# Optimization experiments

Measured on AMD Instinct MI355X. Metric: run time of the kernel, lower is better.

Reference implementation:

```python
import jax, jax.numpy as jnp
import numpy as np

NUM_HEADS = 4
NUM_POINTS = 8


def setup_inputs() -> dict:
    key0 = jax.random.key(0)
    ks = jax.random.split(key0, 14)
    B, S, N, D, C = 1, 6, 10000, 4, 128
    Hf, Wf = 46, 80
    M = Hf * Wf
    HP2 = NUM_HEADS * NUM_POINTS * 2
    HP = NUM_HEADS * NUM_POINTS
    inp = {
        "query": jax.random.normal(ks[0], (B, N, C), jnp.float32),
        "key": jax.random.normal(ks[1], (S, M, B, C), jnp.float32),
        "value": jax.random.normal(ks[2], (S, M, B, C), jnp.float32),
        "query_pos": jax.random.normal(ks[3], (B, N, C), jnp.float32),
        "reference_points_cam": jax.random.uniform(ks[4], (S, B, N, D, 2), jnp.float32),
        "Wv": jax.random.normal(ks[5], (C, C), jnp.float32) * 0.02,
        "bv": jnp.zeros((C,), jnp.float32),
        "Wo": jax.random.normal(ks[6], (C, HP2), jnp.float32) * 0.02,
        "bo": jax.random.normal(ks[7], (HP2,), jnp.float32) * 0.5,
        "Wa": jax.random.normal(ks[8], (C, HP), jnp.float32) * 0.02,
        "ba": jnp.zeros((HP,), jnp.float32),
        "Wp": jax.random.normal(ks[9], (C, C), jnp.float32) * 0.02,
        "bp": jnp.zeros((C,), jnp.float32),
        "spatial_shapes": np.array([[Hf, Wf]], dtype=np.int64),
        "bev_mask": jax.random.uniform(ks[10], (S, B, N, D)) < 0.3,
    }
    return inp


def _bilinear_sample(value_hw, loc, Hf, Wf):
    # value_hw: [BS, H, Hf*Wf, Dh]; loc: [BS, L, H, P, 2] normalized to [0,1]
    # grid_sample(align_corners=False, padding=zeros) semantics: ix = x*W - 0.5
    x = loc[..., 0] * Wf - 0.5
    y = loc[..., 1] * Hf - 0.5
    x0 = jnp.floor(x)
    y0 = jnp.floor(y)
    lx = x - x0
    ly = y - y0
    x0i = x0.astype(jnp.int32)
    y0i = y0.astype(jnp.int32)

    BS, L, H, P = x.shape
    Dh = value_hw.shape[-1]

    def gat(xi, yi):
        valid = (xi >= 0) & (xi < Wf) & (yi >= 0) & (yi < Hf)
        idx = jnp.clip(yi, 0, Hf - 1) * Wf + jnp.clip(xi, 0, Wf - 1)  # [BS,L,H,P]
        idx_t = idx.transpose(0, 2, 1, 3).reshape(BS, H, L * P)
        v = jnp.take_along_axis(value_hw, idx_t[..., None], axis=2)  # [BS,H,L*P,Dh]
        v = v.reshape(BS, H, L, P, Dh)
        return v * valid.transpose(0, 2, 1, 3)[..., None]

    def wt(w):  # [BS,L,H,P] -> [BS,H,L,P,1]
        return w.transpose(0, 2, 1, 3)[..., None]

    out = (gat(x0i, y0i) * wt((1 - lx) * (1 - ly))
           + gat(x0i + 1, y0i) * wt(lx * (1 - ly))
           + gat(x0i, y0i + 1) * wt((1 - lx) * ly)
           + gat(x0i + 1, y0i + 1) * wt(lx * ly))
    return out  # [BS,H,L,P,Dh]


def _deform_attn(q, val, ref, Hf, Wf, Wv, bv, Wo, bo, Wa, ba):
    # q: [BS,L,C], val: [BS,M,C], ref: [BS,L,D,2]
    BS, L, C = q.shape
    Dh = C // NUM_HEADS
    D = ref.shape[2]
    value_p = (val @ Wv + bv).reshape(BS, -1, NUM_HEADS, Dh)
    value_hw = value_p.transpose(0, 2, 1, 3)  # [BS,H,M,Dh]

    off = (q @ Wo + bo).reshape(BS, L, NUM_HEADS, NUM_POINTS, 2)
    attw = jax.nn.softmax((q @ Wa + ba).reshape(BS, L, NUM_HEADS, NUM_POINTS), axis=-1)

    normalizer = jnp.array([Wf, Hf], dtype=q.dtype)  # (x_norm, y_norm)
    off = off / normalizer
    # split points into (points_per_Z, num_Z_anchors) and add per-anchor reference
    off = off.reshape(BS, L, NUM_HEADS, NUM_POINTS // D, D, 2)
    loc = ref[:, :, None, None, :, :] + off  # [BS,L,H,P//D,D,2]
    loc = loc.reshape(BS, L, NUM_HEADS, NUM_POINTS, 2)

    sampled = _bilinear_sample(value_hw, loc, Hf, Wf)  # [BS,H,L,P,Dh]
    out = jnp.einsum('bhlpd,blhp->blhd', sampled, attw)
    return out.reshape(BS, L, C)


def reference(query, key, value, query_pos, reference_points_cam,
              Wv, bv, Wo, bo, Wa, ba, Wp, bp, spatial_shapes, bev_mask):
    B, N, C = query.shape
    S, M = key.shape[0], key.shape[1]
    Hf = int(spatial_shapes[0][0])
    Wf = int(spatial_shapes[0][1])

    q = query + query_pos
    # dense equivalent of the per-camera nonzero() rebatch: run deformable
    # attention for every (batch, camera, query), then mask + scatter-add.
    q_bs = jnp.broadcast_to(q[:, None], (B, S, N, C)).reshape(B * S, N, C)
    ref_bs = reference_points_cam.transpose(1, 0, 2, 3, 4).reshape(B * S, N, -1, 2)
    val_bs = value.transpose(2, 0, 1, 3).reshape(B * S, M, C)

    out = _deform_attn(q_bs, val_bs, ref_bs, Hf, Wf, Wv, bv, Wo, bo, Wa, ba)
    out = out.reshape(B, S, N, C)

    mask_q = (bev_mask.sum(-1) > 0)            # [S,B,N] query visible in camera
    mask_q = mask_q.transpose(1, 0, 2)         # [B,S,N]
    slots = jnp.einsum('bsnc,bsn->bnc', out, mask_q.astype(out.dtype))
    count = jnp.maximum(mask_q.sum(1).astype(out.dtype), 1.0)  # [B,N]
    slots = slots / count[..., None]
    # dropout in eval mode is identity
    return slots @ Wp + bp + query
```

## Files before the change

### kernel.cpp

```cpp
#include <hip/hip_runtime.h>


#define S_DIM 6
#define N_DIM 10000
#define C_DIM 128
#define M_DIM 3680
#define H_DIM 4
#define P_DIM 8
#define DH    32
#define HF    46
#define WF    80

#define G_Q   4
#define NENT  (S_DIM * P_DIM * H_DIM)
#define VHW_SHORTS (S_DIM * H_DIM * M_DIM * DH)

__device__ __forceinline__ float bfl(unsigned u) { return __uint_as_float(u << 16); }
__device__ __forceinline__ float bfh(unsigned u) { return __uint_as_float(u & 0xffff0000u); }
__device__ __forceinline__ unsigned short f2bf(float f) {
    unsigned b = __float_as_uint(f);
    b += 0x7FFFu + ((b >> 16) & 1u);
    return (unsigned short)(b >> 16);
}

__global__ __launch_bounds__(256) void vproj_kernel(
    const float* __restrict__ value,
    const float* __restrict__ Wv,
    const float* __restrict__ bv,
    unsigned short* __restrict__ vhw)
{
    const int row0 = blockIdx.x * 32;
    const int t = threadIdx.x;
    const int tc = t & 31, tr = t >> 5;
    const int c0 = tc * 4, r0 = tr * 4;
    __shared__ float vs[32][C_DIM];

    for (int i = t; i < 32 * 32; i += 256) {
        const int row = i >> 5, c4 = (i & 31) * 4;
        *(float4*)&vs[row][c4] =
            *(const float4*)&value[(size_t)(row0 + row) * C_DIM + c4];
    }
    __syncthreads();

    float acc[4][4];
#pragma unroll
    for (int r = 0; r < 4; ++r)
#pragma unroll
        for (int c = 0; c < 4; ++c) acc[r][c] = 0.f;

    for (int k = 0; k < C_DIM; k += 4) {
        const float4 w0 = *(const float4*)&Wv[(k + 0) * C_DIM + c0];
        const float4 w1 = *(const float4*)&Wv[(k + 1) * C_DIM + c0];
        const float4 w2 = *(const float4*)&Wv[(k + 2) * C_DIM + c0];
        const float4 w3 = *(const float4*)&Wv[(k + 3) * C_DIM + c0];
#pragma unroll
        for (int r = 0; r < 4; ++r) {
            const float4 v = *(const float4*)&vs[r0 + r][k];
            acc[r][0] = fmaf(v.x, w0.x, acc[r][0]);
            acc[r][0] = fmaf(v.y, w1.x, acc[r][0]);
            acc[r][0] = fmaf(v.z, w2.x, acc[r][0]);
            acc[r][0] = fmaf(v.w, w3.x, acc[r][0]);
            acc[r][1] = fmaf(v.x, w0.y, acc[r][1]);
            acc[r][1] = fmaf(v.y, w1.y, acc[r][1]);
            acc[r][1] = fmaf(v.z, w2.y, acc[r][1]);
            acc[r][1] = fmaf(v.w, w3.y, acc[r][1]);
            acc[r][2] = fmaf(v.x, w0.z, acc[r][2]);
            acc[r][2] = fmaf(v.y, w1.z, acc[r][2]);
            acc[r][2] = fmaf(v.z, w2.z, acc[r][2]);
            acc[r][2] = fmaf(v.w, w3.z, acc[r][2]);
            acc[r][3] = fmaf(v.x, w0.w, acc[r][3]);
            acc[r][3] = fmaf(v.y, w1.w, acc[r][3]);
            acc[r][3] = fmaf(v.z, w2.w, acc[r][3]);
            acc[r][3] = fmaf(v.w, w3.w, acc[r][3]);
        }
    }

    const float4 bb = *(const float4*)&bv[c0];
    const int h = c0 >> 5, dh0 = c0 & 31;
#pragma unroll
    for (int r = 0; r < 4; ++r) {
        const int row = row0 + r0 + r;
        const int s = row / M_DIM, m = row - s * M_DIM;
        ushort4 o;
        o.x = f2bf(acc[r][0] + bb.x);
        o.y = f2bf(acc[r][1] + bb.y);
        o.z = f2bf(acc[r][2] + bb.z);
        o.w = f2bf(acc[r][3] + bb.w);
        *(ushort4*)&vhw[(((size_t)s * H_DIM + h) * M_DIM + m) * DH + dh0] = o;
    }
}

__global__ __launch_bounds__(256, 4) void attn_kernel(
    const unsigned short* __restrict__ vhw,
    const float* __restrict__ query,
    const float* __restrict__ query_pos,
    const float* __restrict__ Wo, const float* __restrict__ bo,
    const float* __restrict__ Wa, const float* __restrict__ ba,
    const float* __restrict__ refpts,
    const void* __restrict__ bev_mask,
    const void* __restrict__ sshapes,
    const float* __restrict__ Wp, const float* __restrict__ bp,
    float* __restrict__ out)
{
    const int n0 = blockIdx.x * G_Q;
    const int t = threadIdx.x;

    __shared__ float  qs[G_Q][C_DIM];
    __shared__ float  s_offr[G_Q][64];
    __shared__ float  s_attw[G_Q][32];
    __shared__ uint2  s_pixd[G_Q][S_DIM][P_DIM][H_DIM];
    __shared__ uint2  s_wbd[G_Q][S_DIM][P_DIM][H_DIM];
    __shared__ float  s_slots[G_Q][C_DIM];
    __shared__ int    s_mask[G_Q][S_DIM];
    __shared__ float  s_inv[G_Q];

    for (int i = t; i < G_Q * C_DIM; i += 256) {
        const int g = i >> 7, c = i & 127;
        const size_t a = (size_t)(n0 + g) * C_DIM + c;
        qs[g][c] = query[a] + query_pos[a];
    }
    if (t < G_Q * S_DIM) {
        const int g = t / S_DIM, s = t - g * S_DIM;
        const int n = n0 + g;
        const int* ss32 = (const int*)sshapes;
        const bool i32mode = (ss32[1] == WF);
        int mk;
        if (i32mode) {
            const int* bm = (const int*)bev_mask + ((size_t)s * N_DIM + n) * 4;
            mk = (bm[0] | bm[1] | bm[2] | bm[3]) ? 1 : 0;
        } else {
            const unsigned char* bm =
                (const unsigned char*)bev_mask + ((size_t)s * N_DIM + n) * 4;
            mk = (bm[0] | bm[1] | bm[2] | bm[3]) ? 1 : 0;
        }
        s_mask[g][s] = mk;
    }
    __syncthreads();
    if (t < G_Q) {
        int c = 0;
#pragma unroll
        for (int s = 0; s < S_DIM; ++s) c += s_mask[t][s];
        s_inv[t] = 1.f / fmaxf((float)c, 1.f);
    }

    {
        const int g = t >> 6, j = t & 63;
        float acc = 0.f;
        for (int k = 0; k < C_DIM; k += 4) {
            const float4 q4 = *(const float4*)&qs[g][k];
            acc = fmaf(q4.x, Wo[(k + 0) * 64 + j], acc);
            acc = fmaf(q4.y, Wo[(k + 1) * 64 + j], acc);
            acc = fmaf(q4.z, Wo[(k + 2) * 64 + j], acc);
            acc = fmaf(q4.w, Wo[(k + 3) * 64 + j], acc);
        }
        s_offr[g][j] = acc + bo[j];
    }
    if (t < G_Q * 32) {
        const int g = t >> 5, jj = t & 31;
        float ar = 0.f;
        for (int k = 0; k < C_DIM; k += 4) {
            const float4 q4 = *(const float4*)&qs[g][k];
            ar = fmaf(q4.x, Wa[(k + 0) * 32 + jj], ar);
            ar = fmaf(q4.y, Wa[(k + 1) * 32 + jj], ar);
            ar = fmaf(q4.z, Wa[(k + 2) * 32 + jj], ar);
            ar = fmaf(q4.w, Wa[(k + 3) * 32 + jj], ar);
        }
        ar += ba[jj];
        float m = ar;
        for (int d = 1; d < 8; d <<= 1) m = fmaxf(m, __shfl_xor(m, d, 8));
        const float e = expf(ar - m);
        float sum = e;
        for (int d = 1; d < 8; d <<= 1) sum += __shfl_xor(sum, d, 8);
        s_attw[g][jj] = e / sum;
    }
    __syncthreads();

    for (int i = t; i < G_Q * NENT; i += 256) {
        const int g = i / NENT;
        const int e = i - g * NENT;
        const int s = e >> 5;
        const int rem = e & 31;
        const int p = rem >> 2, h = rem & 3;
        const int hp = h * P_DIM + p;
        const int d = p & 3;
        const int n = n0 + g;

        const float aw = s_attw[g][hp];
        const float offx = s_offr[g][hp * 2 + 0] / (float)WF;
        const float offy = s_offr[g][hp * 2 + 1] / (float)HF;
        const float refx = refpts[(((size_t)s * N_DIM + n) * 4 + d) * 2 + 0];
        const float refy = refpts[(((size_t)s * N_DIM + n) * 4 + d) * 2 + 1];

        const float x = (refx + offx) * (float)WF - 0.5f;
        const float y = (refy + offy) * (float)HF - 0.5f;
        const float x0f = floorf(x), y0f = floorf(y);
        const float lx = x - x0f, ly = y - y0f;
        const int x0 = (int)x0f, y0 = (int)y0f;
        const int x1 = x0 + 1, y1 = y0 + 1;

        const bool vx0 = (x0 >= 0) & (x0 < WF);
        const bool vx1 = (x1 >= 0) & (x1 < WF);
        const bool vy0 = (y0 >= 0) & (y0 < HF);
        const bool vy1 = (y1 >= 0) & (y1 < HF);

        const unsigned cx0 = (unsigned)min(max(x0, 0), WF - 1);
        const unsigned cx1 = (unsigned)min(max(x1, 0), WF - 1);
        const unsigned cy0 = (unsigned)min(max(y0, 0), HF - 1);
        const unsigned cy1 = (unsigned)min(max(y1, 0), HF - 1);

        const unsigned p00 = cy0 * WF + cx0;
        const unsigned p10 = cy0 * WF + cx1;
        const unsigned p01 = cy1 * WF + cx0;
        const unsigned p11 = cy1 * WF + cx1;
        s_pixd[g][s][p][h] = make_uint2(p00 | (p10 << 16), p01 | (p11 << 16));

        const float wx0 = 1.f - lx, wy0 = 1.f - ly;
        const float w00 = (vx0 & vy0) ? wx0 * wy0 * aw : 0.f;
        const float w10 = (vx1 & vy0) ? lx  * wy0 * aw : 0.f;
        const float w01 = (vx0 & vy1) ? wx0 * ly  * aw : 0.f;
        const float w11 = (vx1 & vy1) ? lx  * ly  * aw : 0.f;
        s_wbd[g][s][p][h] = make_uint2(
            (unsigned)f2bf(w00) | ((unsigned)f2bf(w10) << 16),
            (unsigned)f2bf(w01) | ((unsigned)f2bf(w11) << 16));
    }
    __syncthreads();

    {
        const char* vb = (const char*)vhw;
        const int g = t >> 6;
        const int lane = t & 63;
        const int h = lane >> 4;
        const int dhp4 = (lane & 15) * 4;
        float accx = 0.f, accy = 0.f;

        for (int s = 0; s < S_DIM; ++s) {
            if (!s_mask[g][s]) continue;
            const char* vbs = vb + (((s * H_DIM + h) * M_DIM) * (DH * 2) + dhp4);
#pragma unroll
            for (int pg = 0; pg < 4; ++pg) {
                const uint2 pa = s_pixd[g][s][pg * 2 + 0][h];
                const uint2 pb = s_pixd[g][s][pg * 2 + 1][h];
                const unsigned u0 = *(const unsigned*)(vbs + ((pa.x <<  6) & 0x3fffc0u));
                const unsigned u1 = *(const unsigned*)(vbs + ((pa.x >> 10) & 0x3fffc0u));
                const unsigned u2 = *(const unsigned*)(vbs + ((pa.y <<  6) & 0x3fffc0u));
                const unsigned u3 = *(const unsigned*)(vbs + ((pa.y >> 10) & 0x3fffc0u));
                const unsigned u4 = *(const unsigned*)(vbs + ((pb.x <<  6) & 0x3fffc0u));
                const unsigned u5 = *(const unsigned*)(vbs + ((pb.x >> 10) & 0x3fffc0u));
                const unsigned u6 = *(const unsigned*)(vbs + ((pb.y <<  6) & 0x3fffc0u));
                const unsigned u7 = *(const unsigned*)(vbs + ((pb.y >> 10) & 0x3fffc0u));
                const uint2 wa = s_wbd[g][s][pg * 2 + 0][h];
                const uint2 wb2 = s_wbd[g][s][pg * 2 + 1][h];
                const float w00 = bfl(wa.x),  w10 = bfh(wa.x);
                const float w01 = bfl(wa.y),  w11 = bfh(wa.y);
                const float x00 = bfl(wb2.x), x10 = bfh(wb2.x);
                const float x01 = bfl(wb2.y), x11 = bfh(wb2.y);
                accx = fmaf(w00, bfl(u0), accx); accy = fmaf(w00, bfh(u0), accy);
                accx = fmaf(w10, bfl(u1), accx); accy = fmaf(w10, bfh(u1), accy);
                accx = fmaf(w01, bfl(u2), accx); accy = fmaf(w01, bfh(u2), accy);
                accx = fmaf(w11, bfl(u3), accx); accy = fmaf(w11, bfh(u3), accy);
                accx = fmaf(x00, bfl(u4), accx); accy = fmaf(x00, bfh(u4), accy);
                accx = fmaf(x10, bfl(u5), accx); accy = fmaf(x10, bfh(u5), accy);
                accx = fmaf(x01, bfl(u6), accx); accy = fmaf(x01, bfh(u6), accy);
                accx = fmaf(x11, bfl(u7), accx); accy = fmaf(x11, bfh(u7), accy);
            }
        }
        const float inv = s_inv[g];
        *(float2*)&s_slots[g][h * 32 + (lane & 15) * 2] =
            make_float2(accx * inv, accy * inv);
    }
    __syncthreads();

    {
        const int c = t & 127, half = t >> 7;
        const int g0 = half * 2;
        float a0 = 0.f, a1 = 0.f;
        for (int k = 0; k < C_DIM; k += 4) {
            const float4 s0 = *(const float4*)&s_slots[g0][k];
            const float4 s1 = *(const float4*)&s_slots[g0 + 1][k];
            const float w0 = Wp[(k + 0) * C_DIM + c];
            const float w1 = Wp[(k + 1) * C_DIM + c];
            const float w2 = Wp[(k + 2) * C_DIM + c];
            const float w3 = Wp[(k + 3) * C_DIM + c];
            a0 = fmaf(s0.x, w0, a0); a1 = fmaf(s1.x, w0, a1);
            a0 = fmaf(s0.y, w1, a0); a1 = fmaf(s1.y, w1, a1);
            a0 = fmaf(s0.z, w2, a0); a1 = fmaf(s1.z, w2, a1);
            a0 = fmaf(s0.w, w3, a0); a1 = fmaf(s1.w, w3, a1);
        }
        const int na = n0 + g0;
        const float bb = bp[c];
        out[(size_t)na * C_DIM + c]       = a0 + bb + query[(size_t)na * C_DIM + c];
        out[(size_t)(na + 1) * C_DIM + c] = a1 + bb + query[(size_t)(na + 1) * C_DIM + c];
    }
}

extern "C" void kernel_launch(void* const* d_in, const int* in_sizes, int n_in,
                              void* d_out, int out_size, void* d_ws, size_t ws_size,
                              hipStream_t stream) {
    const float* query     = (const float*)d_in[0];
    const float* value     = (const float*)d_in[2];
    const float* query_pos = (const float*)d_in[3];
    const float* refpts    = (const float*)d_in[4];
    const float* Wv        = (const float*)d_in[5];
    const float* bv        = (const float*)d_in[6];
    const float* Wo        = (const float*)d_in[7];
    const float* bo        = (const float*)d_in[8];
    const float* Wa        = (const float*)d_in[9];
    const float* ba        = (const float*)d_in[10];
    const float* Wp        = (const float*)d_in[11];
    const float* bp        = (const float*)d_in[12];
    const void*  sshapes   = d_in[13];
    const void*  bev_mask  = d_in[14];

    unsigned short* vhw = (unsigned short*)d_ws;
    float* outp = (float*)d_out;

    hipLaunchKernelGGL(vproj_kernel, dim3((S_DIM * M_DIM) / 32), dim3(256), 0, stream,
                       value, Wv, bv, vhw);
    hipLaunchKernelGGL(attn_kernel, dim3(N_DIM / G_Q), dim3(256), 0, stream,
                       vhw, query, query_pos, Wo, bo, Wa, ba,
                       refpts, bev_mask, sshapes, Wp, bp, outp);
}
```

Baseline: 78.40 us.

## Halve attn block to 128 threads with 4-wide per-thread vectorized work

The attention kernel now runs 128 threads per block instead of 256. Each thread in the sampling loop handles four channels using 8-byte gathers, so half a wavefront serves one query. The offset, attention-weight and output projections are rewritten to compute four outputs per thread with float4 weight loads and vector stores. This aims to cut per-element instruction and load overhead and improve per-thread ILP, at the cost of fewer threads per block, more registers, and an idle half-block during the final projection.

```diff
diff --git a/kernel.cpp b/kernel.cpp
--- a/kernel.cpp
+++ b/kernel.cpp
@@ -90,7 +90,7 @@
     }
 }
 
-__global__ __launch_bounds__(256, 4) void attn_kernel(
+__global__ __launch_bounds__(128, 4) void attn_kernel(
     const unsigned short* __restrict__ vhw,
     const float* __restrict__ query,
     const float* __restrict__ query_pos,
@@ -114,7 +114,7 @@
     __shared__ int    s_mask[G_Q][S_DIM];
     __shared__ float  s_inv[G_Q];
 
-    for (int i = t; i < G_Q * C_DIM; i += 256) {
+    for (int i = t; i < G_Q * C_DIM; i += 128) {
         const int g = i >> 7, c = i & 127;
         const size_t a = (size_t)(n0 + g) * C_DIM + c;
         qs[g][c] = query[a] + query_pos[a];
@@ -143,39 +143,63 @@
         s_inv[t] = 1.f / fmaxf((float)c, 1.f);
     }
 
-    {
-        const int g = t >> 6, j = t & 63;
-        float acc = 0.f;
+    if (t < 64) {
+        const int g = t >> 4, j0 = (t & 15) * 4;
+        float a0 = 0.f, a1 = 0.f, a2 = 0.f, a3 = 0.f;
         for (int k = 0; k < C_DIM; k += 4) {
             const float4 q4 = *(const float4*)&qs[g][k];
-            acc = fmaf(q4.x, Wo[(k + 0) * 64 + j], acc);
-            acc = fmaf(q4.y, Wo[(k + 1) * 64 + j], acc);
-            acc = fmaf(q4.z, Wo[(k + 2) * 64 + j], acc);
-            acc = fmaf(q4.w, Wo[(k + 3) * 64 + j], acc);
-        }
-        s_offr[g][j] = acc + bo[j];
-    }
-    if (t < G_Q * 32) {
-        const int g = t >> 5, jj = t & 31;
-        float ar = 0.f;
+            float4 w;
+            w = *(const float4*)&Wo[(k + 0) * 64 + j0];
+            a0 = fmaf(q4.x, w.x, a0); a1 = fmaf(q4.x, w.y, a1);
+            a2 = fmaf(q4.x, w.z, a2); a3 = fmaf(q4.x, w.w, a3);
+            w = *(const float4*)&Wo[(k + 1) * 64 + j0];
+            a0 = fmaf(q4.y, w.x, a0); a1 = fmaf(q4.y, w.y, a1);
+            a2 = fmaf(q4.y, w.z, a2); a3 = fmaf(q4.y, w.w, a3);
+            w = *(const float4*)&Wo[(k + 2) * 64 + j0];
+            a0 = fmaf(q4.z, w.x, a0); a1 = fmaf(q4.z, w.y, a1);
+            a2 = fmaf(q4.z, w.z, a2); a3 = fmaf(q4.z, w.w, a3);
+            w = *(const float4*)&Wo[(k + 3) * 64 + j0];
+            a0 = fmaf(q4.w, w.x, a0); a1 = fmaf(q4.w, w.y, a1);
+            a2 = fmaf(q4.w, w.z, a2); a3 = fmaf(q4.w, w.w, a3);
+        }
+        const float4 b4 = *(const float4*)&bo[j0];
+        float4 r; r.x = a0 + b4.x; r.y = a1 + b4.y; r.z = a2 + b4.z; r.w = a3 + b4.w;
+        *(float4*)&s_offr[g][j0] = r;
+    } else {
+        const int i = t - 64;
+        const int g = i >> 3, j0 = (i & 7) * 4;
+        float a0 = 0.f, a1 = 0.f, a2 = 0.f, a3 = 0.f;
         for (int k = 0; k < C_DIM; k += 4) {
             const float4 q4 = *(const float4*)&qs[g][k];
-            ar = fmaf(q4.x, Wa[(k + 0) * 32 + jj], ar);
-            ar = fmaf(q4.y, Wa[(k + 1) * 32 + jj], ar);
-            ar = fmaf(q4.z, Wa[(k + 2) * 32 + jj], ar);
-            ar = fmaf(q4.w, Wa[(k + 3) * 32 + jj], ar);
-        }
-        ar += ba[jj];
-        float m = ar;
-        for (int d = 1; d < 8; d <<= 1) m = fmaxf(m, __shfl_xor(m, d, 8));
-        const float e = expf(ar - m);
-        float sum = e;
-        for (int d = 1; d < 8; d <<= 1) sum += __shfl_xor(sum, d, 8);
-        s_attw[g][jj] = e / sum;
-    }
-    __syncthreads();
-
-    for (int i = t; i < G_Q * NENT; i += 256) {
+            float4 w;
+            w = *(const float4*)&Wa[(k + 0) * 32 + j0];
+            a0 = fmaf(q4.x, w.x, a0); a1 = fmaf(q4.x, w.y, a1);
+            a2 = fmaf(q4.x, w.z, a2); a3 = fmaf(q4.x, w.w, a3);
+            w = *(const float4*)&Wa[(k + 1) * 32 + j0];
+            a0 = fmaf(q4.y, w.x, a0); a1 = fmaf(q4.y, w.y, a1);
+            a2 = fmaf(q4.y, w.z, a2); a3 = fmaf(q4.y, w.w, a3);
+            w = *(const float4*)&Wa[(k + 2) * 32 + j0];
+            a0 = fmaf(q4.z, w.x, a0); a1 = fmaf(q4.z, w.y, a1);
+            a2 = fmaf(q4.z, w.z, a2); a3 = fmaf(q4.z, w.w, a3);
+            w = *(const float4*)&Wa[(k + 3) * 32 + j0];
+            a0 = fmaf(q4.w, w.x, a0); a1 = fmaf(q4.w, w.y, a1);
+            a2 = fmaf(q4.w, w.z, a2); a3 = fmaf(q4.w, w.w, a3);
+        }
+        const float4 b4 = *(const float4*)&ba[j0];
+        a0 += b4.x; a1 += b4.y; a2 += b4.z; a3 += b4.w;
+        float m4 = fmaxf(fmaxf(a0, a1), fmaxf(a2, a3));
+        const float m8 = fmaxf(m4, __shfl_xor(m4, 1));
+        const float e0 = expf(a0 - m8), e1 = expf(a1 - m8);
+        const float e2 = expf(a2 - m8), e3 = expf(a3 - m8);
+        float s4 = e0 + e1 + e2 + e3;
+        const float s8 = s4 + __shfl_xor(s4, 1);
+        const float rs = 1.f / s8;
+        float4 r; r.x = e0 * rs; r.y = e1 * rs; r.z = e2 * rs; r.w = e3 * rs;
+        *(float4*)&s_attw[g][j0] = r;
+    }
+    __syncthreads();
+
+    for (int i = t; i < G_Q * NENT; i += 128) {
         const int g = i / NENT;
         const int e = i - g * NENT;
         const int s = e >> 5;
@@ -227,69 +251,100 @@
 
     {
         const char* vb = (const char*)vhw;
-        const int g = t >> 6;
+        const int w = t >> 6;
         const int lane = t & 63;
-        const int h = lane >> 4;
-        const int dhp4 = (lane & 15) * 4;
-        float accx = 0.f, accy = 0.f;
+        const int q = (w << 1) | (lane >> 5);
+        const int l32 = lane & 31;
+        const int h = l32 >> 3;
+        const int dq8 = (l32 & 7) * 8;
+        float a0 = 0.f, a1 = 0.f, a2 = 0.f, a3 = 0.f;
 
         for (int s = 0; s < S_DIM; ++s) {
-            if (!s_mask[g][s]) continue;
-            const char* vbs = vb + (((s * H_DIM + h) * M_DIM) * (DH * 2) + dhp4);
+            if (!s_mask[q][s]) continue;
+            const char* vbs = vb + (((s * H_DIM + h) * M_DIM) * (DH * 2) + dq8);
 #pragma unroll
             for (int pg = 0; pg < 4; ++pg) {
-                const uint2 pa = s_pixd[g][s][pg * 2 + 0][h];
-                const uint2 pb = s_pixd[g][s][pg * 2 + 1][h];
-                const unsigned u0 = *(const unsigned*)(vbs + ((pa.x <<  6) & 0x3fffc0u));
-                const unsigned u1 = *(const unsigned*)(vbs + ((pa.x >> 10) & 0x3fffc0u));
-                const unsigned u2 = *(const unsigned*)(vbs + ((pa.y <<  6) & 0x3fffc0u));
-                const unsigned u3 = *(const unsigned*)(vbs + ((pa.y >> 10) & 0x3fffc0u));
-                const unsigned u4 = *(const unsigned*)(vbs + ((pb.x <<  6) & 0x3fffc0u));
-                const unsigned u5 = *(const unsigned*)(vbs + ((pb.x >> 10) & 0x3fffc0u));
-                const unsigned u6 = *(const unsigned*)(vbs + ((pb.y <<  6) & 0x3fffc0u));
-                const unsigned u7 = *(const unsigned*)(vbs + ((pb.y >> 10) & 0x3fffc0u));
-                const uint2 wa = s_wbd[g][s][pg * 2 + 0][h];
-                const uint2 wb2 = s_wbd[g][s][pg * 2 + 1][h];
-                const float w00 = bfl(wa.x),  w10 = bfh(wa.x);
-                const float w01 = bfl(wa.y),  w11 = bfh(wa.y);
-                const float x00 = bfl(wb2.x), x10 = bfh(wb2.x);
-                const float x01 = bfl(wb2.y), x11 = bfh(wb2.y);
-                accx = fmaf(w00, bfl(u0), accx); accy = fmaf(w00, bfh(u0), accy);
-                accx = fmaf(w10, bfl(u1), accx); accy = fmaf(w10, bfh(u1), accy);
-                accx = fmaf(w01, bfl(u2), accx); accy = fmaf(w01, bfh(u2), accy);
-                accx = fmaf(w11, bfl(u3), accx); accy = fmaf(w11, bfh(u3), accy);
-                accx = fmaf(x00, bfl(u4), accx); accy = fmaf(x00, bfh(u4), accy);
-                accx = fmaf(x10, bfl(u5), accx); accy = fmaf(x10, bfh(u5), accy);
-                accx = fmaf(x01, bfl(u6), accx); accy = fmaf(x01, bfh(u6), accy);
-                accx = fmaf(x11, bfl(u7), accx); accy = fmaf(x11, bfh(u7), accy);
+                const uint2 pa = s_pixd[q][s][pg * 2 + 0][h];
+                const uint2 pb = s_pixd[q][s][pg * 2 + 1][h];
+                const uint2 u0 = *(const uint2*)(vbs + ((pa.x <<  6) & 0x3fffc0u));
+                const uint2 u1 = *(const uint2*)(vbs + ((pa.x >> 10) & 0x3fffc0u));
+                const uint2 u2 = *(const uint2*)(vbs + ((pa.y <<  6) & 0x3fffc0u));
+                const uint2 u3 = *(const uint2*)(vbs + ((pa.y >> 10) & 0x3fffc0u));
+                const uint2 u4 = *(const uint2*)(vbs + ((pb.x <<  6) & 0x3fffc0u));
+                const uint2 u5 = *(const uint2*)(vbs + ((pb.x >> 10) & 0x3fffc0u));
+                const uint2 u6 = *(const uint2*)(vbs + ((pb.y <<  6) & 0x3fffc0u));
+                const uint2 u7 = *(const uint2*)(vbs + ((pb.y >> 10) & 0x3fffc0u));
+                const uint2 wa = s_wbd[q][s][pg * 2 + 0][h];
+                const uint2 wb = s_wbd[q][s][pg * 2 + 1][h];
+                const float w00 = bfl(wa.x), w10 = bfh(wa.x);
+                const float w01 = bfl(wa.y), w11 = bfh(wa.y);
+                const float x00 = bfl(wb.x), x10 = bfh(wb.x);
+                const float x01 = bfl(wb.y), x11 = bfh(wb.y);
+                a0 = fmaf(w00, bfl(u0.x), a0); a1 = fmaf(w00, bfh(u0.x), a1);
+                a2 = fmaf(w00, bfl(u0.y), a2); a3 = fmaf(w00, bfh(u0.y), a3);
+                a0 = fmaf(w10, bfl(u1.x), a0); a1 = fmaf(w10, bfh(u1.x), a1);
+                a2 = fmaf(w10, bfl(u1.y), a2); a3 = fmaf(w10, bfh(u1.y), a3);
+                a0 = fmaf(w01, bfl(u2.x), a0); a1 = fmaf(w01, bfh(u2.x), a1);
+                a2 = fmaf(w01, bfl(u2.y), a2); a3 = fmaf(w01, bfh(u2.y), a3);
+                a0 = fmaf(w11, bfl(u3.x), a0); a1 = fmaf(w11, bfh(u3.x), a1);
+                a2 = fmaf(w11, bfl(u3.y), a2); a3 = fmaf(w11, bfh(u3.y), a3);
+                a0 = fmaf(x00, bfl(u4.x), a0); a1 = fmaf(x00, bfh(u4.x), a1);
+                a2 = fmaf(x00, bfl(u4.y), a2); a3 = fmaf(x00, bfh(u4.y), a3);
+                a0 = fmaf(x10, bfl(u5.x), a0); a1 = fmaf(x10, bfh(u5.x), a1);
+                a2 = fmaf(x10, bfl(u5.y), a2); a3 = fmaf(x10, bfh(u5.y), a3);
+                a0 = fmaf(x01, bfl(u6.x), a0); a1 = fmaf(x01, bfh(u6.x), a1);
+                a2 = fmaf(x01, bfl(u6.y), a2); a3 = fmaf(x01, bfh(u6.y), a3);
+                a0 = fmaf(x11, bfl(u7.x), a0); a1 = fmaf(x11, bfh(u7.x), a1);
+                a2 = fmaf(x11, bfl(u7.y), a2); a3 = fmaf(x11, bfh(u7.y), a3);
             }
         }
-        const float inv = s_inv[g];
-        *(float2*)&s_slots[g][h * 32 + (lane & 15) * 2] =
-            make_float2(accx * inv, accy * inv);
-    }
-    __syncthreads();
-
-    {
-        const int c = t & 127, half = t >> 7;
-        const int g0 = half * 2;
-        float a0 = 0.f, a1 = 0.f;
+        const float inv = s_inv[q];
+        float4 r; r.x = a0 * inv; r.y = a1 * inv; r.z = a2 * inv; r.w = a3 * inv;
+        *(float4*)&s_slots[q][h * 32 + (l32 & 7) * 4] = r;
+    }
+    __syncthreads();
+
+    if (t < 64) {
+        const int cq = (t & 31) * 4, qp = t >> 5;
+        const int g0 = qp * 2;
+        float a0[4] = {0.f, 0.f, 0.f, 0.f};
+        float a1[4] = {0.f, 0.f, 0.f, 0.f};
         for (int k = 0; k < C_DIM; k += 4) {
             const float4 s0 = *(const float4*)&s_slots[g0][k];
             const float4 s1 = *(const float4*)&s_slots[g0 + 1][k];
-            const float w0 = Wp[(k + 0) * C_DIM + c];
-            const float w1 = Wp[(k + 1) * C_DIM + c];
-            const float w2 = Wp[(k + 2) * C_DIM + c];
-            const float w3 = Wp[(k + 3) * C_DIM + c];
-            a0 = fmaf(s0.x, w0, a0); a1 = fmaf(s1.x, w0, a1);
-            a0 = fmaf(s0.y, w1, a0); a1 = fmaf(s1.y, w1, a1);
-            a0 = fmaf(s0.z, w2, a0); a1 = fmaf(s1.z, w2, a1);
-            a0 = fmaf(s0.w, w3, a0); a1 = fmaf(s1.w, w3, a1);
-        }
+            float4 w;
+            w = *(const float4*)&Wp[(k + 0) * C_DIM + cq];
+            a0[0] = fmaf(s0.x, w.x, a0[0]); a0[1] = fmaf(s0.x, w.y, a0[1]);
+            a0[2] = fmaf(s0.x, w.z, a0[2]); a0[3] = fmaf(s0.x, w.w, a0[3]);
+            a1[0] = fmaf(s1.x, w.x, a1[0]); a1[1] = fmaf(s1.x, w.y, a1[1]);
+            a1[2] = fmaf(s1.x, w.z, a1[2]); a1[3] = fmaf(s1.x, w.w, a1[3]);
+            w = *(const float4*)&Wp[(k + 1) * C_DIM + cq];
+            a0[0] = fmaf(s0.y, w.x, a0[0]); a0[1] = fmaf(s0.y, w.y, a0[1]);
+            a0[2] = fmaf(s0.y, w.z, a0[2]); a0[3] = fmaf(s0.y, w.w, a0[3]);
+            a1[0] = fmaf(s1.y, w.x, a1[0]); a1[1] = fmaf(s1.y, w.y, a1[1]);
+            a1[2] = fmaf(s1.y, w.z, a1[2]); a1[3] = fmaf(s1.y, w.w, a1[3]);
+            w = *(const float4*)&Wp[(k + 2) * C_DIM + cq];
+            a0[0] = fmaf(s0.z, w.x, a0[0]); a0[1] = fmaf(s0.z, w.y, a0[1]);
+            a0[2] = fmaf(s0.z, w.z, a0[2]); a0[3] = fmaf(s0.z, w.w, a0[3]);
+            a1[0] = fmaf(s1.z, w.x, a1[0]); a1[1] = fmaf(s1.z, w.y, a1[1]);
+            a1[2] = fmaf(s1.z, w.z, a1[2]); a1[3] = fmaf(s1.z, w.w, a1[3]);
+            w = *(const float4*)&Wp[(k + 3) * C_DIM + cq];
+            a0[0] = fmaf(s0.w, w.x, a0[0]); a0[1] = fmaf(s0.w, w.y, a0[1]);
+            a0[2] = fmaf(s0.w, w.z, a0[2]); a0[3] = fmaf(s0.w, w.w, a0[3]);
+            a1[0] = fmaf(s1.w, w.x, a1[0]); a1[1] = fmaf(s1.w, w.y, a1[1]);
+            a1[2] = fmaf(s1.w, w.z, a1[2]); a1[3] = fmaf(s1.w, w.w, a1[3]);
+        }
+        const float4 bb = *(const float4*)&bp[cq];
         const int na = n0 + g0;
-        const float bb = bp[c];
-        out[(size_t)na * C_DIM + c]       = a0 + bb + query[(size_t)na * C_DIM + c];
-        out[(size_t)(na + 1) * C_DIM + c] = a1 + bb + query[(size_t)(na + 1) * C_DIM + c];
+        const float4 q0 = *(const float4*)&query[(size_t)na * C_DIM + cq];
+        const float4 q1 = *(const float4*)&query[(size_t)(na + 1) * C_DIM + cq];
+        float4 o0, o1;
+        o0.x = a0[0] + bb.x + q0.x; o0.y = a0[1] + bb.y + q0.y;
+        o0.z = a0[2] + bb.z + q0.z; o0.w = a0[3] + bb.w + q0.w;
+        o1.x = a1[0] + bb.x + q1.x; o1.y = a1[1] + bb.y + q1.y;
+        o1.z = a1[2] + bb.z + q1.z; o1.w = a1[3] + bb.w + q1.w;
+        *(float4*)&out[(size_t)na * C_DIM + cq]       = o0;
+        *(float4*)&out[(size_t)(na + 1) * C_DIM + cq] = o1;
     }
 }
 
@@ -316,7 +371,7 @@
 
     hipLaunchKernelGGL(vproj_kernel, dim3((S_DIM * M_DIM) / 32), dim3(256), 0, stream,
                        value, Wv, bv, vhw);
-    hipLaunchKernelGGL(attn_kernel, dim3(N_DIM / G_Q), dim3(256), 0, stream,
+    hipLaunchKernelGGL(attn_kernel, dim3(N_DIM / G_Q), dim3(128), 0, stream,
                        vhw, query, query_pos, Wo, bo, Wa, ba,
                        refpts, bev_mask, sshapes, Wp, bp, outp);
 }
```

Measured after the change: 98.77 us. 26.0% more time.
